# Performance work log

Measured on AMD Instinct MI355X. Metric: run time of the kernel, lower is better.

The kernel has to match this reference:

```python
import jax, jax.numpy as jnp
import numpy as np

EMBED_DIM = 1024
N_HEADS = 16
HEAD_DIM = EMBED_DIM // N_HEADS
MAX_REL_POS = 2  # hardcoded in the torch module


def _rel_index(length_q, length_k):
    # final_mat[i, j] = clip(i - j, -p, p) + p  with i over k-range, j over q-range
    rq = jnp.arange(length_q)[None, :]
    rk = jnp.arange(length_k)[:, None]
    dist = jnp.clip(rk - rq, -MAX_REL_POS, MAX_REL_POS) + MAX_REL_POS
    return dist  # (len_k, len_q) int; square when len_q == len_k


def setup_inputs() -> dict:
    key = jax.random.key(0)
    ks = jax.random.split(key, 16)
    B, S, E, H, D = 4, 1024, EMBED_DIM, N_HEADS, HEAD_DIM
    xavier = lambda k, shape: jax.random.uniform(
        k, shape, jnp.float32, -1.0, 1.0) * np.sqrt(6.0 / (shape[0] + shape[1]))
    return {
        "query": jax.random.normal(ks[0], (B, S, E), jnp.float32),
        "key": jax.random.normal(ks[1], (B, S, E), jnp.float32),
        "value": jax.random.normal(ks[2], (B, S, E), jnp.float32),
        "Wq": xavier(ks[3], (E, E)), "bq": jnp.zeros((E,), jnp.float32),
        "Wk": xavier(ks[4], (E, E)), "bk": jnp.zeros((E,), jnp.float32),
        "Wv": xavier(ks[5], (E, E)), "bv": jnp.zeros((E,), jnp.float32),
        "Wo": xavier(ks[6], (E, E)), "bo": jnp.zeros((E,), jnp.float32),
        "rpk_table": xavier(ks[7], (2 * MAX_REL_POS + 1, D)),
        "rpv_table": xavier(ks[8], (2 * MAX_REL_POS + 1, D)),
    }


def reference(query, key, value, Wq, bq, Wk, bk, Wv, bv, Wo, bo, rpk_table, rpv_table):
    B, S, E = query.shape
    H, D = N_HEADS, HEAD_DIM
    q = query @ Wq.T + bq
    _k = key @ Wk.T + bk      # computed but unused (faithful to source bug)
    v = value @ Wv.T + bv

    qh = q.reshape(B, S, H, D).transpose(0, 2, 1, 3)   # b h s d
    vh = v.reshape(B, S, H, D).transpose(0, 2, 1, 3)

    # NOTE: source uses query for both sides of the dot product
    dots = jnp.einsum('bhqd,bhkd->bhqk', qh, qh)

    idx = _rel_index(S, S)                              # (S, S)
    rpk = rpk_table[idx]                                # (S, S, D)
    rp_dots = jnp.einsum('bhqd,qkd->bhqk', qh, rpk)

    scale = jnp.sqrt(jnp.asarray(D, q.dtype))
    attn = jax.nn.softmax((dots + rp_dots) / scale, axis=-1)

    weight1 = jnp.einsum('bhqk,bhkd->bhqd', attn, vh)
    rpv = rpv_table[idx]                                # (S, S, D)
    weight2 = jnp.einsum('bhqk,qkd->bhqd', attn, rpv)

    out = (weight1 + weight2).transpose(0, 2, 1, 3).reshape(B, S, E)
    return out @ Wo.T + bo
```

## Files before the change

### kernel.cpp

```cpp
#include <hip/hip_runtime.h>


typedef _Float16 v8h __attribute__((ext_vector_type(8)));
typedef _Float16 v4h __attribute__((ext_vector_type(4)));
typedef float    v4f __attribute__((ext_vector_type(4)));

#define MFMA_F16(A_, B_, C_) __builtin_amdgcn_mfma_f32_16x16x32_f16(A_, B_, C_, 0, 0, 0)

__device__ __forceinline__ void async_copy16(const void* g, void* l) {
    __builtin_amdgcn_global_load_lds(
        (const __attribute__((address_space(1))) void*)g,
        (__attribute__((address_space(3))) void*)l, 16, 0, 0);
}

__device__ __forceinline__ v8h cat4(v4h a, v4h b) {
    return __builtin_shufflevector(a, b, 0, 1, 2, 3, 4, 5, 6, 7);
}

__global__ __launch_bounds__(256) void cvt5_kernel(
    const float* __restrict__ s0, const float* __restrict__ s1,
    const float* __restrict__ s2, const float* __restrict__ s3,
    const float* __restrict__ s4,
    _Float16* __restrict__ d0, _Float16* __restrict__ d1,
    _Float16* __restrict__ d2, _Float16* __restrict__ d3,
    _Float16* __restrict__ d4,
    int n0, int n1, int n2, int n3, int n4)
{
    const float* s; _Float16* d; int n;
    switch (blockIdx.y) {
        case 0:  s = s0; d = d0; n = n0; break;
        case 1:  s = s1; d = d1; n = n1; break;
        case 2:  s = s2; d = d2; n = n2; break;
        case 3:  s = s3; d = d3; n = n3; break;
        default: s = s4; d = d4; n = n4; break;
    }
    int i = (blockIdx.x * 256 + threadIdx.x) * 4;
    if (i >= n) return;
    float4 f = *(const float4*)(s + i);
    v4h o = { (_Float16)f.x, (_Float16)f.y, (_Float16)f.z, (_Float16)f.w };
    *(v4h*)(d + i) = o;
}

template<int TM, int MODE>
__device__ __forceinline__ void gemm_core(const _Float16* __restrict__ A,
                                          const _Float16* __restrict__ W,
                                          const float* __restrict__ bias,
                                          void* __restrict__ outp,
                                          int row0, int col0)
{
    constexpr int WCOLS = (TM == 128) ? 64 : 32;
    constexpr int NJ = WCOLS / 16;
    constexpr int CH = WCOLS / 8;
    constexpr int SC_H = (MODE == 2) ? 4096 : 64 * WCOLS;
    constexpr int STG_H = (TM + 128) * 64;
    constexpr int TOT_H = (STG_H > 4 * SC_H) ? STG_H : 4 * SC_H;
    __shared__ __align__(16) _Float16 smem[TOT_H];
    _Float16* As = smem;
    _Float16* Bs = smem + TM * 64;

    const int tid  = threadIdx.x;
    const int wave = tid >> 6, lane = tid & 63;
    const int quad = lane >> 4, n16 = lane & 15;
    const int wm = (TM == 128) ? (wave >> 1) : 0;
    const int wn = (TM == 128) ? (wave & 1) : wave;
    const int rL = lane >> 3, c8 = lane & 7;
    const int lcs = c8 ^ rL;

    v4f acc[4][NJ] = {};

    for (int kb = 0; kb < 1024; kb += 64) {
        __syncthreads();
        #pragma unroll
        for (int p = 0; p < TM / 32; p++) {
            int rg = wave * (TM / 32) + p;
            int row = rg * 8 + rL;
            async_copy16(A + (size_t)(row0 + row) * 1024 + kb + lcs * 8, &As[rg * 512]);
        }
        #pragma unroll
        for (int p = 0; p < 4; p++) {
            int rg = wave * 4 + p;
            int row = rg * 8 + rL;
            async_copy16(W + (size_t)(col0 + row) * 1024 + kb + lcs * 8, &Bs[rg * 512]);
        }
        __syncthreads();
        #pragma unroll
        for (int ks = 0; ks < 64; ks += 32) {
            const int pc = ((ks >> 3) + quad) ^ (n16 & 7);
            v8h af[4], bf[NJ];
            #pragma unroll
            for (int i = 0; i < 4; i++)
                af[i] = *(const v8h*)(&As[(wm * 64 + i * 16 + n16) * 64 + pc * 8]);
            #pragma unroll
            for (int j = 0; j < NJ; j++)
                bf[j] = *(const v8h*)(&Bs[(wn * WCOLS + j * 16 + n16) * 64 + pc * 8]);
            #pragma unroll
            for (int i = 0; i < 4; i++)
                #pragma unroll
                for (int j = 0; j < NJ; j++)
                    acc[i][j] = MFMA_F16(af[i], bf[j], acc[i][j]);
        }
    }

    __syncthreads();
    const int b     = (row0 + wm * 64) >> 10;
    const int srow0 = (row0 + wm * 64) & 1023;
    const int C0    = col0 + wn * WCOLS;

    if (MODE == 0) {
        _Float16* sc = smem + wave * SC_H;
        #pragma unroll
        for (int i = 0; i < 4; i++)
            #pragma unroll
            for (int j = 0; j < NJ; j++)
                #pragma unroll
                for (int r = 0; r < 4; r++) {
                    int rowL = i * 16 + quad * 4 + r, colL = j * 16 + n16;
                    float v = acc[i][j][r] + bias[C0 + colL];
                    sc[rowL * WCOLS + (((colL >> 3) ^ (rowL & (CH - 1))) << 3) + (colL & 7)] =
                        (_Float16)v;
                }
        int h = C0 >> 6, dbase = C0 & 63;
        #pragma unroll
        for (int it = 0; it < CH; it++) {
            int rowR = it * (64 / CH) + (lane / CH), cR = lane & (CH - 1);
            v8h val = *(const v8h*)(&sc[rowR * WCOLS + ((cR ^ (rowR & (CH - 1))) << 3)]);
            *(v8h*)((_Float16*)outp +
                    (((size_t)(b * 16 + h) * 1024 + srow0 + rowR) << 6) + dbase + cR * 8) = val;
        }
    } else if (MODE == 1) {
        _Float16* sc = smem + wave * SC_H;
        #pragma unroll
        for (int i = 0; i < 4; i++)
            #pragma unroll
            for (int j = 0; j < NJ; j++) {
                int colL = j * 16 + n16;
                int c16 = i * 2 + (quad >> 1);
                v4h pk;
                #pragma unroll
                for (int r = 0; r < 4; r++)
                    pk[r] = (_Float16)(acc[i][j][r] + bias[C0 + colL]);
                *(v4h*)(&sc[colL * 64 + ((c16 ^ (colL & 7)) << 3) + (quad & 1) * 4]) = pk;
            }
        #pragma unroll
        for (int it = 0; it < CH; it++) {
            int dR = it * 8 + (lane >> 3), scn = lane & 7;
            v8h val = *(const v8h*)(&sc[dR * 64 + ((scn ^ (dR & 7)) << 3)]);
            int cg = C0 + dR;
            int h = cg >> 6, dl = cg & 63;
            *(v8h*)((_Float16*)outp +
                    ((size_t)((b * 16 + h) * 64 + dl) << 10) + srow0 + scn * 8) = val;
        }
    } else {
        float* sc = (float*)smem + wave * 2048;
        #pragma unroll
        for (int i = 0; i < 4; i++)
            #pragma unroll
            for (int j = 0; j < 2; j++)
                #pragma unroll
                for (int r = 0; r < 4; r++) {
                    int rowL = i * 16 + quad * 4 + r, colL = j * 16 + n16;
                    sc[rowL * 32 + (((colL >> 2) ^ (rowL & 7)) << 2) + (colL & 3)] =
                        acc[i][j][r] + bias[col0 + wn * 32 + colL];
                }
        #pragma unroll
        for (int it = 0; it < 8; it++) {
            int rowR = it * 8 + (lane >> 3), cR = lane & 7;
            v4f val = *(const v4f*)(&sc[rowR * 32 + ((cR ^ (rowR & 7)) << 2)]);
            *(v4f*)((float*)outp + (size_t)(row0 + rowR) * 1024 + col0 + wn * 32 + cR * 4) = val;
        }
    }
}

__global__ __launch_bounds__(256) void gemm_qv_kernel(
    const _Float16* __restrict__ Aq, const _Float16* __restrict__ Av,
    const _Float16* __restrict__ Wq, const _Float16* __restrict__ Wv,
    const float* __restrict__ bq, const float* __restrict__ bv,
    _Float16* __restrict__ q_out, _Float16* __restrict__ v_out)
{
    int id = blockIdx.x;
    int k8 = id & 7;
    int z  = k8 & 1;
    int y  = (k8 >> 1) * 16 + ((id >> 3) & 15);
    int x  = (id >> 7) & 7;
    if (z) gemm_core<64, 1>(Av, Wv, bv, (void*)v_out, y * 64, x * 128);
    else   gemm_core<64, 0>(Aq, Wq, bq, (void*)q_out, y * 64, x * 128);
}

__global__ __launch_bounds__(256) void gemm_o_kernel(
    const _Float16* __restrict__ A, const _Float16* __restrict__ W,
    const float* __restrict__ bias, float* __restrict__ outp)
{
    int id = blockIdx.x;
    int y = (id & 7) * 8 + ((id >> 3) & 7);
    int x = id >> 6;
    gemm_core<64, 2>(A, W, bias, (void*)outp, y * 64, x * 128);
}

__global__ __launch_bounds__(256) void attn_kernel(
    const _Float16* __restrict__ qb,
    const _Float16* __restrict__ vt,
    const float* __restrict__ rpk, const float* __restrict__ rpv,
    _Float16* __restrict__ attn_o)
{
    const int blk = blockIdx.x;
    const int bh = blk & 63;
    const int q0 = (blk >> 6) * 64;
    const int tid = threadIdx.x;
    const int wave = tid >> 6, lane = tid & 63;
    const int quad = lane >> 4, n16 = lane & 15;
    const int qw = q0 + wave * 16;
    const _Float16* Qh = qb + (size_t)bh * 1024 * 64;
    const _Float16* Vh = vt + (size_t)bh * 64 * 1024;

    __shared__ __align__(16) _Float16 Ks[2][64 * 64];
    __shared__ __align__(16) _Float16 Vs[2][64 * 64];
    __shared__ float rqs[4][16][5];

    const int rL = lane >> 3, c8 = lane & 7;
    const int lcs = c8 ^ rL;

    #pragma unroll
    for (int p = 0; p < 2; p++) {
        int c = wave * 2 + p;
        int row = c * 8 + rL;
        async_copy16(Qh + (size_t)row * 64 + lcs * 8, &Ks[0][c * 512]);
        async_copy16(Vh + (size_t)row * 1024 + lcs * 8, &Vs[0][c * 512]);
    }

    {
        int m = lane >> 2, seg = lane & 3;
        const _Float16* qrow = Qh + (size_t)(qw + m) * 64 + seg * 16;
        v8h qa = *(const v8h*)(qrow);
        v8h qc = *(const v8h*)(qrow + 8);
        float qd[16];
        #pragma unroll
        for (int x = 0; x < 8; x++) { qd[x] = (float)qa[x]; qd[8 + x] = (float)qc[x]; }
        float qq = 0.f;
        #pragma unroll
        for (int x = 0; x < 16; x++) qq += qd[x] * qd[x];
        qq += __shfl_xor(qq, 1);
        qq += __shfl_xor(qq, 2);
        #pragma unroll
        for (int t = 0; t < 5; t++) {
            float s = 0.f;
            #pragma unroll
            for (int x = 0; x < 16; x++) s += qd[x] * rpk[t * 64 + seg * 16 + x];
            s += __shfl_xor(s, 1);
            s += __shfl_xor(s, 2);
            if (seg == 0) rqs[wave][m][t] = (s - qq) * 0.125f;
        }
    }

    v8h aq0 = *(const v8h*)(Qh + (size_t)(qw + n16) * 64 + quad * 8);
    v8h aq1 = *(const v8h*)(Qh + (size_t)(qw + n16) * 64 + 32 + quad * 8);

    __syncthreads();

    float rc[5];
    #pragma unroll
    for (int t = 0; t < 5; t++) rc[t] = rqs[wave][n16][t];

    float bkt[5] = {0.f, 0.f, 0.f, 0.f, 0.f};
    v4f O[4] = {};

    const int pphys0 = quad ^ (n16 & 7);
    const int pphys1 = (quad + 4) ^ (n16 & 7);
    const int xk = n16 & 7;
    const int vq = quad >> 1, vo = (quad & 1) * 4;

    for (int it = 0; it < 16; ++it) {
        const int cur = it & 1;
        const int kb = it * 64;
        if (it + 1 < 16) {
            const int nxt = 1 - cur;
            const int kn = kb + 64;
            #pragma unroll
            for (int p = 0; p < 2; p++) {
                int c = wave * 2 + p;
                int row = c * 8 + rL;
                async_copy16(Qh + (size_t)(kn + row) * 64 + lcs * 8, &Ks[nxt][c * 512]);
                async_copy16(Vh + (size_t)row * 1024 + kn + lcs * 8, &Vs[nxt][c * 512]);
            }
        }

        int pkLo[4], pkHi[4];
        #pragma unroll
        for (int t = 0; t < 4; t++) {
            v8h ak0 = *(const v8h*)(&Ks[cur][(t * 16 + n16) * 64 + pphys0 * 8]);
            v8h ak1 = *(const v8h*)(&Ks[cur][(t * 16 + n16) * 64 + pphys1 * 8]);
            v4f s = {0.f, 0.f, 0.f, 0.f};
            s = MFMA_F16(ak0, aq0, s);
            s = MFMA_F16(ak1, aq1, s);
            const int dqt = qw - kb - t * 16;
            float pv[4];
            if (dqt >= 32) {
                #pragma unroll
                for (int r = 0; r < 4; r++) {
                    float p = __expf(fmaf(s[r], 0.125f, rc[4]));
                    pv[r] = p; bkt[4] += p;
                }
            } else if (dqt <= -32) {
                #pragma unroll
                for (int r = 0; r < 4; r++) {
                    float p = __expf(fmaf(s[r], 0.125f, rc[0]));
                    pv[r] = p; bkt[0] += p;
                }
            } else {
                #pragma unroll
                for (int r = 0; r < 4; r++) {
                    int diff = dqt + n16 - quad * 4 - r;
                    float rv = diff >= 2  ? rc[4]
                             : diff == 1  ? rc[3]
                             : diff == 0  ? rc[2]
                             : diff == -1 ? rc[1]
                                          : rc[0];
                    float p = __expf(fmaf(s[r], 0.125f, rv));
                    pv[r] = p;
                    bkt[4] += (diff >= 2)  ? p : 0.f;
                    bkt[3] += (diff == 1)  ? p : 0.f;
                    bkt[2] += (diff == 0)  ? p : 0.f;
                    bkt[1] += (diff == -1) ? p : 0.f;
                    bkt[0] += (diff <= -2) ? p : 0.f;
                }
            }
            pkLo[t] = __builtin_bit_cast(int, __builtin_amdgcn_cvt_pkrtz(pv[0], pv[1]));
            pkHi[t] = __builtin_bit_cast(int, __builtin_amdgcn_cvt_pkrtz(pv[2], pv[3]));
        }

        union { int d[4]; v8h v; } ub0, ub1;
        ub0.d[0] = pkLo[0]; ub0.d[1] = pkHi[0]; ub0.d[2] = pkLo[1]; ub0.d[3] = pkHi[1];
        ub1.d[0] = pkLo[2]; ub1.d[1] = pkHi[2]; ub1.d[2] = pkLo[3]; ub1.d[3] = pkHi[3];
        v8h bf0 = ub0.v, bf1 = ub1.v;

        #pragma unroll
        for (int dt = 0; dt < 4; dt++) {
            const int rowd = (dt * 16 + n16) * 64;
            v4h a0 = *(const v4h*)(&Vs[cur][rowd + ((vq     ^ xk) << 3) + vo]);
            v4h a1 = *(const v4h*)(&Vs[cur][rowd + (((vq+2) ^ xk) << 3) + vo]);
            v4h a2 = *(const v4h*)(&Vs[cur][rowd + (((vq+4) ^ xk) << 3) + vo]);
            v4h a3 = *(const v4h*)(&Vs[cur][rowd + (((vq+6) ^ xk) << 3) + vo]);
            O[dt] = MFMA_F16(cat4(a0, a1), bf0, O[dt]);
            O[dt] = MFMA_F16(cat4(a2, a3), bf1, O[dt]);
        }

        __syncthreads();
    }

    #pragma unroll
    for (int t = 0; t < 5; t++) {
        bkt[t] += __shfl_xor(bkt[t], 16);
        bkt[t] += __shfl_xor(bkt[t], 32);
    }
    float l = bkt[0] + bkt[1] + bkt[2] + bkt[3] + bkt[4];
    float inv = 1.0f / l;
    int q = qw + n16;
    size_t orow = (size_t)((bh >> 4) * 1024 + q) * 1024 + (bh & 15) * 64;
    #pragma unroll
    for (int dt = 0; dt < 4; dt++) {
        int d0 = dt * 16 + quad * 4;
        v4h st;
        #pragma unroll
        for (int r = 0; r < 4; r++) {
            int d = d0 + r;
            float w2 = bkt[4] * rpv[4 * 64 + d] + bkt[3] * rpv[3 * 64 + d]
                     + bkt[2] * rpv[2 * 64 + d] + bkt[1] * rpv[1 * 64 + d]
                     + bkt[0] * rpv[0 * 64 + d];
            st[r] = (_Float16)((O[dt][r] + w2) * inv);
        }
        *(v4h*)(attn_o + orow + d0) = st;
    }
}

extern "C" void kernel_launch(void* const* d_in, const int* in_sizes, int n_in,
                              void* d_out, int out_size, void* d_ws, size_t ws_size,
                              hipStream_t stream)
{
    const float* query = (const float*)d_in[0];
    const float* value = (const float*)d_in[2];
    const float* Wq = (const float*)d_in[3];
    const float* bq = (const float*)d_in[4];
    const float* Wv = (const float*)d_in[7];
    const float* bv = (const float*)d_in[8];
    const float* Wo = (const float*)d_in[9];
    const float* bo = (const float*)d_in[10];
    const float* rpk = (const float*)d_in[11];
    const float* rpv = (const float*)d_in[12];
    float* out = (float*)d_out;

    char* ws = (char*)d_ws;
    const size_t MB = 1024 * 1024;
    _Float16* q_bhsd = (_Float16*)(ws);
    _Float16* v_t    = (_Float16*)(ws + 8 * MB);
    _Float16* q16    = (_Float16*)(ws + 16 * MB);
    _Float16* attn_o = (_Float16*)(ws + 16 * MB);
    _Float16* v16    = (_Float16*)(ws + 24 * MB);
    _Float16* wq16   = (_Float16*)(ws + 32 * MB);
    _Float16* wv16   = (_Float16*)(ws + 34 * MB);
    _Float16* wo16   = (_Float16*)(ws + 36 * MB);

    cvt5_kernel<<<dim3(4096, 5), 256, 0, stream>>>(
        query, value, Wq, Wv, Wo, q16, v16, wq16, wv16, wo16,
        4096 * 1024, 4096 * 1024, 1024 * 1024, 1024 * 1024, 1024 * 1024);

    gemm_qv_kernel<<<dim3(1024), 256, 0, stream>>>(
        q16, v16, wq16, wv16, bq, bv, q_bhsd, v_t);

    attn_kernel<<<dim3(1024), 256, 0, stream>>>(q_bhsd, v_t, rpk, rpv, attn_o);

    gemm_o_kernel<<<dim3(512), 256, 0, stream>>>(attn_o, wo16, bo, out);
}
```

Measured before the change: 205.7 us.

## Enlarge QV GEMM tiles to 128 rows and permute V layout for vector loads

The QV projection GEMM switches from 64-row to 128-row tiles, halving the grid to 512 blocks and reusing each loaded weight tile across more rows. The V-transpose output is now written in a permuted key order within each 32-key group, so the attention kernel can fetch V operands with two 8-wide LDS loads instead of four 4-wide loads plus shuffles. This trades fewer, larger GEMM blocks (more registers, lower occupancy) and scattered 8-byte global stores for cheaper LDS reads in the attention inner loop.

After: 198.0 us. 3.8% less time.

```diff
diff --git a/kernel.cpp b/kernel.cpp
--- a/kernel.cpp
+++ b/kernel.cpp
@@ -11,10 +11,6 @@
     __builtin_amdgcn_global_load_lds(
         (const __attribute__((address_space(1))) void*)g,
         (__attribute__((address_space(3))) void*)l, 16, 0, 0);
-}
-
-__device__ __forceinline__ v8h cat4(v4h a, v4h b) {
-    return __builtin_shufflevector(a, b, 0, 1, 2, 3, 4, 5, 6, 7);
 }
 
 __global__ __launch_bounds__(256) void cvt5_kernel(
@@ -50,7 +46,6 @@
 {
     constexpr int WCOLS = (TM == 128) ? 64 : 32;
     constexpr int NJ = WCOLS / 16;
-    constexpr int CH = WCOLS / 8;
     constexpr int SC_H = (MODE == 2) ? 4096 : 64 * WCOLS;
     constexpr int STG_H = (TM + 128) * 64;
     constexpr int TOT_H = (STG_H > 4 * SC_H) ? STG_H : 4 * SC_H;
@@ -116,16 +111,15 @@
                 for (int r = 0; r < 4; r++) {
                     int rowL = i * 16 + quad * 4 + r, colL = j * 16 + n16;
                     float v = acc[i][j][r] + bias[C0 + colL];
-                    sc[rowL * WCOLS + (((colL >> 3) ^ (rowL & (CH - 1))) << 3) + (colL & 7)] =
-                        (_Float16)v;
+                    sc[rowL * 64 + (((colL >> 3) ^ (rowL & 7)) << 3) + (colL & 7)] = (_Float16)v;
                 }
-        int h = C0 >> 6, dbase = C0 & 63;
-        #pragma unroll
-        for (int it = 0; it < CH; it++) {
-            int rowR = it * (64 / CH) + (lane / CH), cR = lane & (CH - 1);
-            v8h val = *(const v8h*)(&sc[rowR * WCOLS + ((cR ^ (rowR & (CH - 1))) << 3)]);
+        int h = C0 >> 6;
+        #pragma unroll
+        for (int it = 0; it < 8; it++) {
+            int rowR = it * 8 + (lane >> 3), cR = lane & 7;
+            v8h val = *(const v8h*)(&sc[rowR * 64 + ((cR ^ (rowR & 7)) << 3)]);
             *(v8h*)((_Float16*)outp +
-                    (((size_t)(b * 16 + h) * 1024 + srow0 + rowR) << 6) + dbase + cR * 8) = val;
+                    (((size_t)(b * 16 + h) * 1024 + srow0 + rowR) << 6) + cR * 8) = val;
         }
     } else if (MODE == 1) {
         _Float16* sc = smem + wave * SC_H;
@@ -142,13 +136,20 @@
                 *(v4h*)(&sc[colL * 64 + ((c16 ^ (colL & 7)) << 3) + (quad & 1) * 4]) = pk;
             }
         #pragma unroll
-        for (int it = 0; it < CH; it++) {
-            int dR = it * 8 + (lane >> 3), scn = lane & 7;
-            v8h val = *(const v8h*)(&sc[dR * 64 + ((scn ^ (dR & 7)) << 3)]);
+        for (int it = 0; it < 8; it++) {
+            int dR = it * 8 + (lane >> 3), g = lane & 7;
+            v8h val = *(const v8h*)(&sc[dR * 64 + ((g ^ (dR & 7)) << 3)]);
             int cg = C0 + dR;
             int h = cg >> 6, dl = cg & 63;
-            *(v8h*)((_Float16*)outp +
-                    ((size_t)((b * 16 + h) * 64 + dl) << 10) + srow0 + scn * 8) = val;
+            _Float16* base = (_Float16*)outp +
+                             ((size_t)((b * 16 + h) * 64 + dl) << 10) + srow0;
+            int a4  = ((g >> 1) & 1) * 4, b32 = (g >> 2) * 32;
+            int p0  = b32 + ((2 * g) & 3) * 8 + a4;
+            int p1  = b32 + ((2 * g + 1) & 3) * 8 + a4;
+            v4h lo = __builtin_shufflevector(val, val, 0, 1, 2, 3);
+            v4h hi = __builtin_shufflevector(val, val, 4, 5, 6, 7);
+            *(v4h*)(base + p0) = lo;
+            *(v4h*)(base + p1) = hi;
         }
     } else {
         float* sc = (float*)smem + wave * 2048;
@@ -178,12 +179,11 @@
     _Float16* __restrict__ q_out, _Float16* __restrict__ v_out)
 {
     int id = blockIdx.x;
-    int k8 = id & 7;
-    int z  = k8 & 1;
-    int y  = (k8 >> 1) * 16 + ((id >> 3) & 15);
-    int x  = (id >> 7) & 7;
-    if (z) gemm_core<64, 1>(Av, Wv, bv, (void*)v_out, y * 64, x * 128);
-    else   gemm_core<64, 0>(Aq, Wq, bq, (void*)q_out, y * 64, x * 128);
+    int y = (id & 7) | (((id >> 3) & 3) << 3);
+    int x = (id >> 5) & 7;
+    int z = id >> 8;
+    if (z) gemm_core<128, 1>(Av, Wv, bv, (void*)v_out, y * 128, x * 128);
+    else   gemm_core<128, 0>(Aq, Wq, bq, (void*)q_out, y * 128, x * 128);
 }
 
 __global__ __launch_bounds__(256) void gemm_o_kernel(
@@ -265,8 +265,6 @@
 
     const int pphys0 = quad ^ (n16 & 7);
     const int pphys1 = (quad + 4) ^ (n16 & 7);
-    const int xk = n16 & 7;
-    const int vq = quad >> 1, vo = (quad & 1) * 4;
 
     for (int it = 0; it < 16; ++it) {
         const int cur = it & 1;
@@ -335,12 +333,10 @@
         #pragma unroll
         for (int dt = 0; dt < 4; dt++) {
             const int rowd = (dt * 16 + n16) * 64;
-            v4h a0 = *(const v4h*)(&Vs[cur][rowd + ((vq     ^ xk) << 3) + vo]);
-            v4h a1 = *(const v4h*)(&Vs[cur][rowd + (((vq+2) ^ xk) << 3) + vo]);
-            v4h a2 = *(const v4h*)(&Vs[cur][rowd + (((vq+4) ^ xk) << 3) + vo]);
-            v4h a3 = *(const v4h*)(&Vs[cur][rowd + (((vq+6) ^ xk) << 3) + vo]);
-            O[dt] = MFMA_F16(cat4(a0, a1), bf0, O[dt]);
-            O[dt] = MFMA_F16(cat4(a2, a3), bf1, O[dt]);
+            v8h av0 = *(const v8h*)(&Vs[cur][rowd + pphys0 * 8]);
+            v8h av1 = *(const v8h*)(&Vs[cur][rowd + pphys1 * 8]);
+            O[dt] = MFMA_F16(av0, bf0, O[dt]);
+            O[dt] = MFMA_F16(av1, bf1, O[dt]);
         }
 
         __syncthreads();
@@ -402,7 +398,7 @@
         query, value, Wq, Wv, Wo, q16, v16, wq16, wv16, wo16,
         4096 * 1024, 4096 * 1024, 1024 * 1024, 1024 * 1024, 1024 * 1024);
 
-    gemm_qv_kernel<<<dim3(1024), 256, 0, stream>>>(
+    gemm_qv_kernel<<<dim3(512), 256, 0, stream>>>(
         q16, v16, wq16, wv16, bq, bv, q_bhsd, v_t);
 
     attn_kernel<<<dim3(1024), 256, 0, stream>>>(q_bhsd, v_t, rpk, rpv, attn_o);
```
